# Kernel optimization log

Measured on AMD Instinct MI355X. Metric: run time of the kernel, lower is better.

Reference implementation:

```python
import jax, jax.numpy as jnp
import numpy as np

C = 512
C8 = C // 8  # reduceRate = 8


def setup_inputs() -> dict:
    key = jax.random.key(0)
    ks = jax.random.split(key, 8)
    B, H, W = 4, 64, 64
    x = jax.random.normal(ks[0], (B, C, H, W), dtype=jnp.float32)
    # 1x1 convs == per-pixel linear maps: weight [out, in], bias [out]
    sb = 1.0 / np.sqrt(C)
    Wb = jax.random.uniform(ks[1], (C8, C), jnp.float32, -sb, sb)
    bb = jax.random.uniform(ks[2], (C8,), jnp.float32, -sb, sb)
    Wc = jax.random.uniform(ks[3], (C8, C), jnp.float32, -sb, sb)
    bc = jax.random.uniform(ks[4], (C8,), jnp.float32, -sb, sb)
    Wd = jax.random.uniform(ks[5], (C, C), jnp.float32, -sb, sb)
    bd = jax.random.uniform(ks[6], (C,), jnp.float32, -sb, sb)
    # nn.Parameter(torch.zeros(1)) -> use small nonzero so grads are nontrivial
    alpha = jnp.full((1,), 0.1, dtype=jnp.float32)
    return {"x": x, "Wb": Wb, "bb": bb, "Wc": Wc, "bc": bc,
            "Wd": Wd, "bd": bd, "alpha": alpha}


def reference(x, Wb, bb, Wc, bc, Wd, bd, alpha):
    B, Cin, H, W = x.shape
    N = H * W
    xf = x.reshape(B, Cin, N)                                    # [B,C,N]
    feat_b = jnp.einsum('oc,bcn->bon', Wb, xf) + bb[None, :, None]  # [B,C/8,N]
    feat_c = jnp.einsum('oc,bcn->bon', Wc, xf) + bc[None, :, None]  # [B,C/8,N]
    # attention_s[b,n,m] = softmax_m( b^T c ), unscaled as in source
    attn = jax.nn.softmax(jnp.einsum('bkn,bkm->bnm', feat_b, feat_c), axis=-1)
    feat_d = jnp.einsum('oc,bcn->bon', Wd, xf) + bd[None, :, None]  # [B,C,N]
    # feat_e = feat_d @ attn^T : e[b,c,n] = sum_m d[b,c,m] * attn[b,n,m]
    feat_e = jnp.einsum('bcm,bnm->bcn', feat_d, attn)
    out = (alpha[0] * feat_e).reshape(B, Cin, H, W) + x
    return out
```

## Files before the change

kernel.cpp:

```cpp
#include <hip/hip_runtime.h>
#include <hip/hip_bf16.h>
#include <math.h>

#define BB 4
#define CC 512
#define NN 4096
#define LOG2E 1.4426950408889634f

typedef short short8 __attribute__((ext_vector_type(8)));
typedef float f32x4 __attribute__((ext_vector_type(4)));
typedef float f32x16 __attribute__((ext_vector_type(16)));

#define MFMA16(a, b, c) __builtin_amdgcn_mfma_f32_16x16x32_bf16((a), (b), (c), 0, 0, 0)
#define MFMA32(a, b, c) __builtin_amdgcn_mfma_f32_32x32x16_bf16((a), (b), (c), 0, 0, 0)

static __device__ __forceinline__ unsigned short f2bf(float f) {
    union { float f; unsigned int u; } v; v.f = f;
    unsigned int r = v.u + 0x7FFFu + ((v.u >> 16) & 1u);
    return (unsigned short)(r >> 16);
}

static __device__ __forceinline__ unsigned int pk2bf(float a, float b) {
    __hip_bfloat162 t = __float22bfloat162_rn(make_float2(a, b));
    return *(unsigned int*)&t;
}

static __device__ __forceinline__ void gload16(const void* g, void* l) {
    __builtin_amdgcn_global_load_lds(
        (const __attribute__((address_space(1))) unsigned int*)g,
        (__attribute__((address_space(3))) unsigned int*)l, 16, 0, 0);
}

__global__ __launch_bounds__(256) void k_wconv(
    const float* __restrict__ Wb, const float* __restrict__ bb,
    const float* __restrict__ Wc, const float* __restrict__ bc,
    const float* __restrict__ Wd, const float* __restrict__ bd,
    unsigned short* __restrict__ Wcat, float* __restrict__ bcat)
{
    int r = blockIdx.x;
    int t = threadIdx.x;
    const float* src; const float* bsrc; int bi; float scale;
    if (r < 64)       { src = Wb + (size_t)r * 512;         bsrc = bb; bi = r;       scale = LOG2E; }
    else if (r < 128) { src = Wc + (size_t)(r - 64) * 512;  bsrc = bc; bi = r - 64;  scale = 1.0f; }
    else              { src = Wd + (size_t)(r - 128) * 512; bsrc = bd; bi = r - 128; scale = 1.0f; }
    float2 v = *(const float2*)&src[t * 2];
    *(unsigned int*)&Wcat[(size_t)r * 512 + t * 2] = pk2bf(v.x * scale, v.y * scale);
    if (t == 0) bcat[r] = bsrc[bi] * scale;
}

__global__ __launch_bounds__(256) void k_transpose(
    const float* __restrict__ x, unsigned short* __restrict__ xT)
{
    __shared__ float lds[64][65];
    int bid = blockIdx.x;
    int cb = bid & 7;
    int nb = (bid >> 3) & 63;
    int b  = bid >> 9;
    int t = threadIdx.x;
    int r = t >> 4;
    int q = t & 15;

#pragma unroll
    for (int p = 0; p < 4; ++p) {
        int c = p * 16 + r;
        const float4 v = *(const float4*)&x[((size_t)(b * CC + cb * 64 + c)) * NN + nb * 64 + q * 4];
        lds[c][q * 4 + 0] = v.x;
        lds[c][q * 4 + 1] = v.y;
        lds[c][q * 4 + 2] = v.z;
        lds[c][q * 4 + 3] = v.w;
    }
    __syncthreads();
#pragma unroll
    for (int p = 0; p < 4; ++p) {
        int n = p * 16 + r;
        ushort4 o;
        o.x = f2bf(lds[q * 4 + 0][n]);
        o.y = f2bf(lds[q * 4 + 1][n]);
        o.z = f2bf(lds[q * 4 + 2][n]);
        o.w = f2bf(lds[q * 4 + 3][n]);
        *(ushort4*)&xT[((size_t)(b * NN + nb * 64 + n)) * CC + cb * 64 + q * 4] = o;
    }
}

__global__ __launch_bounds__(256) void k_feat(
    const unsigned short* __restrict__ xT,
    const unsigned short* __restrict__ Wcat,
    const float* __restrict__ bcat,
    unsigned short* __restrict__ Q,
    unsigned short* __restrict__ Kf,
    unsigned short* __restrict__ Vtl)
{
    int bid = blockIdx.x;
    int ob = bid % 10;
    int nb = (bid / 10) & 63;
    int b  = bid / 640;
    int t = threadIdx.x, w = t >> 6, lane = t & 63;
    int lr = lane & 15, lg = lane >> 4;

    int o_local = w * 16 + lr;
    int wr = (ob == 0) ? o_local : (ob == 1 ? 64 + o_local : 128 + (ob - 2) * 64 + o_local);
    const unsigned short* Wrow = Wcat + (size_t)wr * CC;
    const unsigned short* xrow = xT + ((size_t)(b * NN + nb * 64)) * CC;

    f32x4 acc[4] = {};

    for (int kt = 0; kt < 8; ++kt) {
        int k0 = kt * 64;
        short8 bfr[2];
#pragma unroll
        for (int ks = 0; ks < 2; ++ks)
            bfr[ks] = *(const short8*)&Wrow[k0 + ks * 32 + lg * 8];
#pragma unroll
        for (int rf = 0; rf < 4; ++rf) {
#pragma unroll
            for (int ks = 0; ks < 2; ++ks) {
                short8 a = *(const short8*)&xrow[(size_t)(rf * 16 + lr) * CC + k0 + ks * 32 + lg * 8];
                acc[rf] = MFMA16(a, bfr[ks], acc[rf]);
            }
        }
    }

    float bias = bcat[wr];
#pragma unroll
    for (int rf = 0; rf < 4; ++rf) {
        if (ob < 2) {
            unsigned short* dst = (ob == 0) ? Q : Kf;
#pragma unroll
            for (int i = 0; i < 4; ++i) {
                int n = nb * 64 + rf * 16 + lg * 4 + i;
                dst[((size_t)(b * NN + n)) * 64 + o_local] = f2bf(acc[rf][i] + bias);
            }
        } else {
            int row = (ob - 2) * 64 + o_local;
            int nl = rf * 16 + lg * 4;
            ushort4 o4;
            o4.x = f2bf(acc[rf][0] + bias);
            o4.y = f2bf(acc[rf][1] + bias);
            o4.z = f2bf(acc[rf][2] + bias);
            o4.w = f2bf(acc[rf][3] + bias);
            *(ushort4*)&Vtl[(((size_t)(b * 64 + nb)) * CC + row) * 64 + nl] = o4;
        }
    }
}

__global__ __launch_bounds__(256, 2) void k_attn(
    const unsigned short* __restrict__ Q,
    const unsigned short* __restrict__ Kf,
    const unsigned short* __restrict__ Vtl,
    const float* __restrict__ x,
    const float* __restrict__ alpha_p,
    float* __restrict__ out)
{
    __shared__ __align__(16) char smem[2][32768];
    __shared__ float Lacc[2][64];

    int bid0 = blockIdx.x;
    int bid = (bid0 & 7) * 64 + (bid0 >> 3);
    int cb = bid & 1;
    int qb = (bid >> 1) & 63;
    int b  = bid >> 7;
    int tid = threadIdx.x;
    int w = tid >> 6, lane = tid & 63;
    int l31 = lane & 31, h = lane >> 5;
    int qi = w >> 1, mi = w & 1;

    const char* Vb = (const char*)Vtl + (size_t)b * (64 * 65536) + (size_t)cb * 32768;
    const unsigned short* Kb = Kf + (size_t)b * NN * 64;

    short8 qfr[4];
    {
        const unsigned short* qp = Q + ((size_t)b * NN + qb * 64 + qi * 32 + l31) * 64;
#pragma unroll
        for (int kk = 0; kk < 4; ++kk)
            qfr[kk] = *(const short8*)&qp[kk * 16 + h * 8];
    }

    int vbase[2];
#pragma unroll
    for (int kk = 0; kk < 2; ++kk)
        vbase[kk] = (l31 * 128 + mi * 64 + kk * 32 + h * 16) ^ ((l31 & 7) << 4);

#define STAGE(T, BUF)                                                          \
    do {                                                                       \
        const char* vs_ = Vb + (size_t)(T) * 65536;                            \
        _Pragma("unroll")                                                      \
        for (int i_ = 0; i_ < 8; ++i_) {                                       \
            int du_ = (i_ * 4 + w) * 1024;                                     \
            int dl_ = du_ + lane * 16;                                         \
            int sl_ = dl_ ^ (((dl_ >> 7) & 7) << 4);                           \
            gload16(vs_ + sl_, &smem[BUF][0] + du_);                           \
        }                                                                      \
    } while (0)

#define KLOAD(DST, T)                                                          \
    do {                                                                       \
        const unsigned short* kp_ = Kb + ((size_t)(T) * 64 + mi * 32 + l31) * 64; \
        _Pragma("unroll")                                                      \
        for (int kk_ = 0; kk_ < 4; ++kk_)                                      \
            DST[kk_] = *(const short8*)&kp_[kk_ * 16 + h * 8];                 \
    } while (0)

    f32x16 acc[8] = {};
    float lsum = 0.f;
    short8 kfA[4], kfB[4];

    STAGE(0, 0);
    KLOAD(kfA, 0);
    asm volatile("s_waitcnt vmcnt(0)" ::: "memory");
    __builtin_amdgcn_s_barrier();

#define BODY(T, BUF, KF)                                                       \
    do {                                                                       \
        f32x16 st = {};                                                        \
        __builtin_amdgcn_s_setprio(1);                                         \
        _Pragma("unroll")                                                      \
        for (int kk = 0; kk < 4; ++kk)                                         \
            st = MFMA32(KF[kk], qfr[kk], st);                                  \
        __builtin_amdgcn_s_setprio(0);                                         \
        float p[16];                                                           \
        _Pragma("unroll")                                                      \
        for (int e = 0; e < 16; ++e) {                                         \
            p[e] = __builtin_amdgcn_exp2f(st[e]);                              \
            lsum += p[e];                                                      \
        }                                                                      \
        unsigned int pk[4][2];                                                 \
        _Pragma("unroll")                                                      \
        for (int tt = 0; tt < 4; ++tt)                                         \
            _Pragma("unroll")                                                  \
            for (int pp = 0; pp < 2; ++pp)                                     \
                pk[tt][pp] = pk2bf(p[4 * tt + 2 * pp], p[4 * tt + 2 * pp + 1]);\
        short8 pfrag[2];                                                       \
        _Pragma("unroll")                                                      \
        for (int kk = 0; kk < 2; ++kk) {                                       \
            unsigned int sel0 = h ? pk[2 * kk][0] : pk[2 * kk + 1][0];         \
            unsigned int sel1 = h ? pk[2 * kk][1] : pk[2 * kk + 1][1];         \
            unsigned int r0 = __shfl_xor(sel0, 32);                            \
            unsigned int r1 = __shfl_xor(sel1, 32);                            \
            union { unsigned int u[4]; short8 s; } pa;                         \
            pa.u[0] = h ? r0 : pk[2 * kk][0];                                  \
            pa.u[1] = h ? r1 : pk[2 * kk][1];                                  \
            pa.u[2] = h ? pk[2 * kk + 1][0] : r0;                              \
            pa.u[3] = h ? pk[2 * kk + 1][1] : r1;                              \
            pfrag[kk] = pa.s;                                                  \
        }                                                                      \
        const char* vb_ = &smem[BUF][0];                                       \
        __builtin_amdgcn_s_setprio(1);                                         \
        _Pragma("unroll")                                                      \
        for (int ct = 0; ct < 8; ++ct) {                                       \
            short8 vf0 = *(const short8*)(vb_ + ct * 4096 + vbase[0]);         \
            short8 vf1 = *(const short8*)(vb_ + ct * 4096 + vbase[1]);         \
            acc[ct] = MFMA32(vf0, pfrag[0], acc[ct]);                          \
            acc[ct] = MFMA32(vf1, pfrag[1], acc[ct]);                          \
        }                                                                      \
        __builtin_amdgcn_s_setprio(0);                                         \
        asm volatile("s_waitcnt vmcnt(0)" ::: "memory");                       \
        __builtin_amdgcn_s_barrier();                                          \
    } while (0)

#pragma unroll 1
    for (int t2 = 0; t2 < 32; ++t2) {
        int t0 = t2 * 2;
        STAGE(t0 + 1, 1);
        KLOAD(kfB, t0 + 1);
        BODY(t0, 0, kfA);
        int nt = (t0 + 2 < 64) ? t0 + 2 : 63;
        STAGE(nt, 0);
        KLOAD(kfA, nt);
        BODY(t0 + 1, 1, kfB);
    }

    lsum += __shfl_xor(lsum, 32);
    if (h == 0) Lacc[mi][qi * 32 + l31] = lsum;
    __syncthreads();

    float* red = (float*)&smem[0][0];
    {
        int region = qi * 2 + (1 - mi);
#pragma unroll
        for (int c2 = 0; c2 < 4; ++c2)
            *(f32x16*)(red + region * 4096 + c2 * 1024 + lane * 16) = acc[(1 - mi) * 4 + c2];
    }
    __syncthreads();

    float alpha = alpha_p[0];
    float inv = alpha / (Lacc[0][qi * 32 + l31] + Lacc[1][qi * 32 + l31]);
    int myreg = qi * 2 + mi;
#pragma unroll
    for (int c2 = 0; c2 < 4; ++c2) {
        f32x16 o = acc[mi * 4 + c2] + *(const f32x16*)(red + myreg * 4096 + c2 * 1024 + lane * 16);
        int cbase = cb * 256 + (mi * 4 + c2) * 32;
#pragma unroll
        for (int r = 0; r < 16; ++r) {
            int row = cbase + (r & 3) + 8 * (r >> 2) + 4 * h;
            size_t off = ((size_t)(b * CC + row)) * NN + qb * 64 + qi * 32 + l31;
            out[off] = x[off] + o[r] * inv;
        }
    }
#undef BODY
#undef KLOAD
#undef STAGE
}

extern "C" void kernel_launch(void* const* d_in, const int* in_sizes, int n_in,
                              void* d_out, int out_size, void* d_ws, size_t ws_size,
                              hipStream_t stream)
{
    const float* x     = (const float*)d_in[0];
    const float* Wb    = (const float*)d_in[1];
    const float* bbias = (const float*)d_in[2];
    const float* Wc    = (const float*)d_in[3];
    const float* cbias = (const float*)d_in[4];
    const float* Wd    = (const float*)d_in[5];
    const float* dbias = (const float*)d_in[6];
    const float* alpha = (const float*)d_in[7];
    float* out = (float*)d_out;

    unsigned short* xT   = (unsigned short*)d_ws;
    unsigned short* Qd   = xT + (size_t)BB * NN * CC;
    unsigned short* Kd   = Qd + (size_t)BB * NN * 64;
    unsigned short* Vtl  = Kd + (size_t)BB * NN * 64;
    unsigned short* Wcat = Vtl + (size_t)BB * NN * CC;
    float*          bcat = (float*)(Wcat + (size_t)640 * 512);

    k_wconv<<<640, 256, 0, stream>>>(Wb, bbias, Wc, cbias, Wd, dbias, Wcat, bcat);
    k_transpose<<<2048, 256, 0, stream>>>(x, xT);
    k_feat<<<2560, 256, 0, stream>>>(xT, Wcat, bcat, Qd, Kd, Vtl);
    k_attn<<<512, 256, 0, stream>>>(Qd, Kd, Vtl, x, alpha, out);
}
```

Baseline: 334.7 us.

## Stage x tile in LDS for feature GEMM, regroup K layout, vectorize epilogue

k_feat now copies the 64x512 bf16 x tile into swizzled LDS once per block and reads MFMA operands from there, where before each wave read them from global memory. K is written in a fragment-grouped layout so k_attn can load K fragments with contiguous loads. The PV MFMA operand order is swapped so each lane holds four consecutive query positions, which lets the epilogue use float4 loads of x and float4 stores of out instead of scalar strided accesses. The 64KB LDS tile per block limits k_feat occupancy.

After: 280.0 us. 16.4% less time.

```diff
diff --git a/kernel.cpp b/kernel.cpp
--- a/kernel.cpp
+++ b/kernel.cpp
@@ -82,39 +82,55 @@
     }
 }
 
-__global__ __launch_bounds__(256) void k_feat(
+__global__ __launch_bounds__(256, 2) void k_feat(
     const unsigned short* __restrict__ xT,
     const unsigned short* __restrict__ Wcat,
     const float* __restrict__ bcat,
     unsigned short* __restrict__ Q,
-    unsigned short* __restrict__ Kf,
+    unsigned short* __restrict__ Kg,
     unsigned short* __restrict__ Vtl)
 {
+    __shared__ __align__(16) unsigned short xs[64 * 512];
     int bid = blockIdx.x;
     int ob = bid % 10;
     int nb = (bid / 10) & 63;
     int b  = bid / 640;
-    int t = threadIdx.x, w = t >> 6, lane = t & 63;
+    int tid = threadIdx.x, w = tid >> 6, lane = tid & 63;
     int lr = lane & 15, lg = lane >> 4;
+
+    {
+        const char* xbase = (const char*)(xT + ((size_t)(b * NN + nb * 64)) * CC);
+#pragma unroll
+        for (int i = 0; i < 16; ++i) {
+            int du = i * 4096 + w * 1024;
+            int dl = du + lane * 16;
+            int row = dl >> 10, within = dl & 1023;
+            gload16(xbase + row * 1024 + (within ^ ((row & 7) << 4)),
+                    (char*)&xs[0] + du);
+        }
+    }
+    asm volatile("s_waitcnt vmcnt(0)" ::: "memory");
+    __syncthreads();
 
     int o_local = w * 16 + lr;
     int wr = (ob == 0) ? o_local : (ob == 1 ? 64 + o_local : 128 + (ob - 2) * 64 + o_local);
     const unsigned short* Wrow = Wcat + (size_t)wr * CC;
-    const unsigned short* xrow = xT + ((size_t)(b * NN + nb * 64)) * CC;
 
     f32x4 acc[4] = {};
 
     for (int kt = 0; kt < 8; ++kt) {
-        int k0 = kt * 64;
         short8 bfr[2];
 #pragma unroll
         for (int ks = 0; ks < 2; ++ks)
-            bfr[ks] = *(const short8*)&Wrow[k0 + ks * 32 + lg * 8];
+            bfr[ks] = *(const short8*)&Wrow[kt * 64 + ks * 32 + lg * 8];
 #pragma unroll
         for (int rf = 0; rf < 4; ++rf) {
+            int row = rf * 16 + lr;
 #pragma unroll
             for (int ks = 0; ks < 2; ++ks) {
-                short8 a = *(const short8*)&xrow[(size_t)(rf * 16 + lr) * CC + k0 + ks * 32 + lg * 8];
+                int kbyte = kt * 128 + ks * 64 + lg * 16;
+                short8 a = *(const short8*)((const char*)&xs[0] + row * 1024 +
+                                            (kbyte ^ ((row & 7) << 4)));
                 acc[rf] = MFMA16(a, bfr[ks], acc[rf]);
             }
         }
@@ -123,12 +139,19 @@
     float bias = bcat[wr];
 #pragma unroll
     for (int rf = 0; rf < 4; ++rf) {
-        if (ob < 2) {
-            unsigned short* dst = (ob == 0) ? Q : Kf;
+        if (ob == 0) {
 #pragma unroll
             for (int i = 0; i < 4; ++i) {
                 int n = nb * 64 + rf * 16 + lg * 4 + i;
-                dst[((size_t)(b * NN + n)) * 64 + o_local] = f2bf(acc[rf][i] + bias);
+                Q[((size_t)(b * NN + n)) * 64 + o_local] = f2bf(acc[rf][i] + bias);
+            }
+        } else if (ob == 1) {
+            int d = o_local;
+            size_t base = ((((size_t)(b * 64 + nb) * 4 + (d >> 4)) * 2 + ((d >> 3) & 1)) * 64) * 8 + (d & 7);
+#pragma unroll
+            for (int i = 0; i < 4; ++i) {
+                int m = rf * 16 + lg * 4 + i;
+                Kg[base + (size_t)m * 8] = f2bf(acc[rf][i] + bias);
             }
         } else {
             int row = (ob - 2) * 64 + o_local;
@@ -145,7 +168,7 @@
 
 __global__ __launch_bounds__(256, 2) void k_attn(
     const unsigned short* __restrict__ Q,
-    const unsigned short* __restrict__ Kf,
+    const unsigned short* __restrict__ Kg,
     const unsigned short* __restrict__ Vtl,
     const float* __restrict__ x,
     const float* __restrict__ alpha_p,
@@ -165,7 +188,7 @@
     int qi = w >> 1, mi = w & 1;
 
     const char* Vb = (const char*)Vtl + (size_t)b * (64 * 65536) + (size_t)cb * 32768;
-    const unsigned short* Kb = Kf + (size_t)b * NN * 64;
+    const unsigned short* Kb = Kg + (size_t)b * 64 * 4096;
 
     short8 qfr[4];
     {
@@ -175,10 +198,10 @@
             qfr[kk] = *(const short8*)&qp[kk * 16 + h * 8];
     }
 
-    int vbase[2];
+    int pb[2];
 #pragma unroll
     for (int kk = 0; kk < 2; ++kk)
-        vbase[kk] = (l31 * 128 + mi * 64 + kk * 32 + h * 16) ^ ((l31 & 7) << 4);
+        pb[kk] = (l31 * 128 + mi * 64 + kk * 32 + h * 16) ^ ((l31 & 7) << 4);
 
 #define STAGE(T, BUF)                                                          \
     do {                                                                       \
@@ -194,10 +217,11 @@
 
 #define KLOAD(DST, T)                                                          \
     do {                                                                       \
-        const unsigned short* kp_ = Kb + ((size_t)(T) * 64 + mi * 32 + l31) * 64; \
+        const unsigned short* kp_ = Kb + (size_t)(T) * 4096 +                  \
+            (size_t)(h) * 512 + (size_t)(mi * 32 + l31) * 8;                   \
         _Pragma("unroll")                                                      \
         for (int kk_ = 0; kk_ < 4; ++kk_)                                      \
-            DST[kk_] = *(const short8*)&kp_[kk_ * 16 + h * 8];                 \
+            DST[kk_] = *(const short8*)&kp_[kk_ * 1024];                       \
     } while (0)
 
     f32x16 acc[8] = {};
@@ -209,7 +233,7 @@
     asm volatile("s_waitcnt vmcnt(0)" ::: "memory");
     __builtin_amdgcn_s_barrier();
 
-#define BODY(T, BUF, KF)                                                       \
+#define BODY(BUF, KF)                                                          \
     do {                                                                       \
         f32x16 st = {};                                                        \
         __builtin_amdgcn_s_setprio(1);                                         \
@@ -247,10 +271,10 @@
         __builtin_amdgcn_s_setprio(1);                                         \
         _Pragma("unroll")                                                      \
         for (int ct = 0; ct < 8; ++ct) {                                       \
-            short8 vf0 = *(const short8*)(vb_ + ct * 4096 + vbase[0]);         \
-            short8 vf1 = *(const short8*)(vb_ + ct * 4096 + vbase[1]);         \
-            acc[ct] = MFMA32(vf0, pfrag[0], acc[ct]);                          \
-            acc[ct] = MFMA32(vf1, pfrag[1], acc[ct]);                          \
+            short8 vf0 = *(const short8*)(vb_ + ct * 4096 + pb[0]);            \
+            short8 vf1 = *(const short8*)(vb_ + ct * 4096 + pb[1]);            \
+            acc[ct] = MFMA32(pfrag[0], vf0, acc[ct]);                          \
+            acc[ct] = MFMA32(pfrag[1], vf1, acc[ct]);                          \
         }                                                                      \
         __builtin_amdgcn_s_setprio(0);                                         \
         asm volatile("s_waitcnt vmcnt(0)" ::: "memory");                       \
@@ -262,38 +286,56 @@
         int t0 = t2 * 2;
         STAGE(t0 + 1, 1);
         KLOAD(kfB, t0 + 1);
-        BODY(t0, 0, kfA);
+        BODY(0, kfA);
         int nt = (t0 + 2 < 64) ? t0 + 2 : 63;
         STAGE(nt, 0);
         KLOAD(kfA, nt);
-        BODY(t0 + 1, 1, kfB);
+        BODY(1, kfB);
     }
 
     lsum += __shfl_xor(lsum, 32);
     if (h == 0) Lacc[mi][qi * 32 + l31] = lsum;
+
+    float* red = (float*)&smem[0][0];
     __syncthreads();
-
-    float* red = (float*)&smem[0][0];
     {
         int region = qi * 2 + (1 - mi);
-#pragma unroll
-        for (int c2 = 0; c2 < 4; ++c2)
-            *(f32x16*)(red + region * 4096 + c2 * 1024 + lane * 16) = acc[(1 - mi) * 4 + c2];
+        float* dst = red + region * 4096 + lane * 16;
+        if (mi == 0) {
+#pragma unroll
+            for (int c2 = 0; c2 < 4; ++c2) *(f32x16*)(dst + c2 * 1024) = acc[4 + c2];
+        } else {
+#pragma unroll
+            for (int c2 = 0; c2 < 4; ++c2) *(f32x16*)(dst + c2 * 1024) = acc[c2];
+        }
     }
     __syncthreads();
 
     float alpha = alpha_p[0];
-    float inv = alpha / (Lacc[0][qi * 32 + l31] + Lacc[1][qi * 32 + l31]);
-    int myreg = qi * 2 + mi;
+    const float* srcr = red + (qi * 2 + mi) * 4096 + lane * 16;
 #pragma unroll
     for (int c2 = 0; c2 < 4; ++c2) {
-        f32x16 o = acc[mi * 4 + c2] + *(const f32x16*)(red + myreg * 4096 + c2 * 1024 + lane * 16);
-        int cbase = cb * 256 + (mi * 4 + c2) * 32;
-#pragma unroll
-        for (int r = 0; r < 16; ++r) {
-            int row = cbase + (r & 3) + 8 * (r >> 2) + 4 * h;
-            size_t off = ((size_t)(b * CC + row)) * NN + qb * 64 + qi * 32 + l31;
-            out[off] = x[off] + o[r] * inv;
+        f32x16 o = (mi == 0 ? acc[c2] : acc[4 + c2]) + *(const f32x16*)(srcr + c2 * 1024);
+        int ctg = mi * 4 + c2;
+        int c = cb * 256 + ctg * 32 + l31;
+#pragma unroll
+        for (int rg = 0; rg < 4; ++rg) {
+            int qloc = qi * 32 + rg * 8 + h * 4;
+            float4 l0 = *(const float4*)&Lacc[0][qloc];
+            float4 l1 = *(const float4*)&Lacc[1][qloc];
+            float4 inv;
+            inv.x = alpha / (l0.x + l1.x);
+            inv.y = alpha / (l0.y + l1.y);
+            inv.z = alpha / (l0.z + l1.z);
+            inv.w = alpha / (l0.w + l1.w);
+            size_t off = ((size_t)(b * CC + c)) * NN + qb * 64 + qloc;
+            float4 xv = *(const float4*)&x[off];
+            float4 ov;
+            ov.x = xv.x + o[rg * 4 + 0] * inv.x;
+            ov.y = xv.y + o[rg * 4 + 1] * inv.y;
+            ov.z = xv.z + o[rg * 4 + 2] * inv.z;
+            ov.w = xv.w + o[rg * 4 + 3] * inv.w;
+            *(float4*)&out[off] = ov;
         }
     }
 #undef BODY
@@ -317,13 +359,13 @@
 
     unsigned short* xT   = (unsigned short*)d_ws;
     unsigned short* Qd   = xT + (size_t)BB * NN * CC;
-    unsigned short* Kd   = Qd + (size_t)BB * NN * 64;
-    unsigned short* Vtl  = Kd + (size_t)BB * NN * 64;
+    unsigned short* Kgd  = Qd + (size_t)BB * NN * 64;
+    unsigned short* Vtl  = Kgd + (size_t)BB * NN * 64;
     unsigned short* Wcat = Vtl + (size_t)BB * NN * CC;
     float*          bcat = (float*)(Wcat + (size_t)640 * 512);
 
     k_wconv<<<640, 256, 0, stream>>>(Wb, bbias, Wc, cbias, Wd, dbias, Wcat, bcat);
     k_transpose<<<2048, 256, 0, stream>>>(x, xT);
-    k_feat<<<2560, 256, 0, stream>>>(xT, Wcat, bcat, Qd, Kd, Vtl);
-    k_attn<<<512, 256, 0, stream>>>(Qd, Kd, Vtl, x, alpha, out);
-}
+    k_feat<<<2560, 256, 0, stream>>>(xT, Wcat, bcat, Qd, Kgd, Vtl);
+    k_attn<<<512, 256, 0, stream>>>(Qd, Kgd, Vtl, x, alpha, out);
+}
```
